# Kernel optimization log

Hardware: AMD Instinct MI355X
Metric: run time of the kernel (lower is better)

The kernel has to match this reference:

```python
import jax, jax.numpy as jnp
import numpy as np
from jax import lax

KERNEL_SIZE = 3  # matches init_kwargs


def setup_inputs() -> dict:
    key = jax.random.key(0)
    heatmap = jax.random.normal(key, (8, 16, 512, 512), dtype=jnp.float32)
    return {"heatmap": heatmap, "max_peaks": 262144}


def reference(heatmap, max_peaks):
    """Peak detection: local maxima of 3x3 neighborhood that are > 0.

    Returns:
      peaks:  (B, max_peaks, 3) float32, rows [x, y, confidence] packed in
              (channel, row-major) order (identical ordering to the torch
              per-channel torch.where + cat), zero-padded after counts[b].
      counts: (B,) int32, number of valid peak rows per batch item.
    """
    k = KERNEL_SIZE
    pad = (k - 1) // 2
    # max_pool2d(stride=1, padding=pad) pads with -inf implicitly
    max_pooled = lax.reduce_window(
        heatmap, -jnp.inf, lax.max,
        window_dimensions=(1, 1, k, k),
        window_strides=(1, 1, 1, 1),
        padding=[(0, 0), (0, 0), (pad, pad), (pad, pad)],
    )
    peak_mask = (heatmap == max_pooled) & (heatmap > 0)

    B, C, H, W = heatmap.shape
    n = C * H * W
    flat_mask = peak_mask.reshape(B, n)
    flat_val = heatmap.reshape(B, n)

    # Stream compaction: stable argsort moves valid flat indices (in order)
    # to the front; invalid entries get sentinel key n.
    idx = jnp.arange(n, dtype=jnp.int32)
    keys = jnp.where(flat_mask, idx, jnp.int32(n))
    order = jnp.argsort(keys, axis=1)[:, :max_peaks]  # (B, max_peaks)

    valid = jnp.take_along_axis(flat_mask, order, axis=1)
    conf = jnp.take_along_axis(flat_val, order, axis=1)
    x = (order % W).astype(heatmap.dtype)
    y = ((order // W) % H).astype(heatmap.dtype)

    peaks = jnp.where(valid[..., None], jnp.stack([x, y, conf], axis=-1), 0.0)
    counts = flat_mask.sum(axis=1).astype(jnp.int32)
    return peaks, counts
```

## Files before the change

### kernel.cpp

```cpp
#include <hip/hip_runtime.h>


namespace {
constexpr int kB = 8;
constexpr int kC = 16;
constexpr int kH = 512;
constexpr int kW = 512;
constexpr int kNPB = kC * kH * kW;
constexpr int kMaxPeaks = 262144;
constexpr int kRows = 8;
constexpr int kStripsPerBatch = kC * (kH / kRows);
constexpr int kNStrips = kB * kStripsPerBatch;
constexpr int kWPB = 4;
constexpr int kTPB = 64 * kWPB;
constexpr int kCap = kRows * kW;
constexpr long long kPeaksElems = (long long)kB * kMaxPeaks * 3;
constexpr float kNeg = -3.402823466e38f;
}

__device__ __forceinline__ float fmax3(float a, float b, float c) {
  return fmaxf(fmaxf(a, b), c);
}

__device__ __forceinline__ void loadrow(const float* __restrict__ rp, int y0,
                                        int i, float d[8]) {
  const int yy = y0 + i;
  if (yy >= 0 && yy < kH) {
    const float4 q0 = *reinterpret_cast<const float4*>(rp + i * kW);
    const float4 q1 = *reinterpret_cast<const float4*>(rp + i * kW + 4);
    d[0] = q0.x; d[1] = q0.y; d[2] = q0.z; d[3] = q0.w;
    d[4] = q1.x; d[5] = q1.y; d[6] = q1.z; d[7] = q1.w;
  } else {
#pragma unroll
    for (int j = 0; j < 8; ++j) d[j] = kNeg;
  }
}


__global__ void __launch_bounds__(kTPB)
peak_record_kernel(const float* __restrict__ hm,
                   unsigned long long* __restrict__ rec,
                   int* __restrict__ cnts) {
  const int t = threadIdx.x, lane = t & 63, wv = t >> 6;
  const int s = blockIdx.x * kWPB + wv;
  const int b = s >> 10;
  const int si = s & 1023;
  const int c = si >> 6;
  const int y0 = (si & 63) * kRows;
  const float* rp = hm + (long long)b * kNPB + c * (kH * kW) + y0 * kW + lane * 8;
  unsigned long long* rb = rec + (long long)s * kCap;

  float A[8], Bv[8], Cv[8], N1[8], N2[8];
  loadrow(rp, y0, -1, A);
  loadrow(rp, y0, 0, Bv);
  loadrow(rp, y0, 1, Cv);
  loadrow(rp, y0, 2, N1);
  loadrow(rp, y0, 3, N2);

  const unsigned long long pm = (lane == 0) ? 0ull : (~0ull >> (64 - lane));
  int rbase = 0;
#pragma unroll
  for (int r = 0; r < kRows; ++r) {
    float cm[8];
#pragma unroll
    for (int j = 0; j < 8; ++j) cm[j] = fmax3(A[j], Bv[j], Cv[j]);
    float hl = __shfl_up(cm[7], 1, 64);
    float hr = __shfl_down(cm[0], 1, 64);
    if (lane == 0) hl = kNeg;
    if (lane == 63) hr = kNeg;
    float m[8];
    m[0] = fmax3(hl, cm[0], cm[1]);
#pragma unroll
    for (int j = 1; j < 7; ++j) m[j] = fmax3(cm[j - 1], cm[j], cm[j + 1]);
    m[7] = fmax3(cm[6], cm[7], hr);

    unsigned long long w[8];
    int lexcl = 0, rowcnt = 0;
#pragma unroll
    for (int j = 0; j < 8; ++j) {
      const float v = Bv[j];
      w[j] = __ballot((v == m[j]) && (v > 0.0f));
      lexcl += (int)__popcll(w[j] & pm);
      rowcnt += (int)__popcll(w[j]);
    }
    int rank = rbase + lexcl;
    const unsigned yx = (unsigned)((y0 + r) << 16);
#pragma unroll
    for (int j = 0; j < 8; ++j) {
      const int f = (int)((w[j] >> lane) & 1);
      if (f) {
        rb[rank] = ((unsigned long long)__float_as_uint(Bv[j]) << 32) |
                   (unsigned long long)(yx | (unsigned)(lane * 8 + j));
      }
      rank += f;
    }
    rbase += rowcnt;

#pragma unroll
    for (int j = 0; j < 8; ++j) { A[j] = Bv[j]; Bv[j] = Cv[j]; Cv[j] = N1[j]; N1[j] = N2[j]; }
    if (r <= 4) loadrow(rp, y0, r + 4, N2);
  }
  if (lane == 0) cnts[s] = rbase;
}

__global__ void __launch_bounds__(kTPB)
peak_scatter_kernel(const unsigned long long* __restrict__ rec,
                    const int* __restrict__ cnts,
                    float* __restrict__ out) {
  __shared__ int s_pre[kWPB], s_tot[kWPB], s_c[kWPB];
  const int t = threadIdx.x, lane = t & 63, wv = t >> 6;
  const int g = blockIdx.x;
  const int b = g >> 8;
  const int g0 = (g & 255) * kWPB;
  const int* cb = cnts + b * kStripsPerBatch;

  const int4 c4 = *reinterpret_cast<const int4*>(cb + t * 4);
  const int idx0 = t * 4;
  int tot = c4.x + c4.y + c4.z + c4.w;
  int pre = (idx0 < g0) ? tot : 0;
  if (idx0 == g0) { s_c[0] = c4.x; s_c[1] = c4.y; s_c[2] = c4.z; s_c[3] = c4.w; }
#pragma unroll
  for (int d = 32; d >= 1; d >>= 1) {
    pre += __shfl_down(pre, d, 64);
    tot += __shfl_down(tot, d, 64);
  }
  if (lane == 0) { s_pre[wv] = pre; s_tot[wv] = tot; }
  __syncthreads();
  const int base = s_pre[0] + s_pre[1] + s_pre[2] + s_pre[3];
  if (g0 == 0 && t == 0)
    out[kPeaksElems + b] =
        (float)(s_tot[0] + s_tot[1] + s_tot[2] + s_tot[3]);

  int off0 = base;
  for (int k = 0; k < wv; ++k) off0 += s_c[k];
  if (off0 >= kMaxPeaks) return;

  const int s = b * kStripsPerBatch + g0 + wv;
  const int lim = min(s_c[wv], kMaxPeaks - off0);
  const unsigned long long* rb = rec + (long long)s * kCap;
  float* o = out + (long long)b * kMaxPeaks * 3 + (long long)off0 * 3;
  for (int i = lane; i < lim; i += 64) {
    const unsigned long long v = rb[i];
    float* p = o + (long long)i * 3;
    p[0] = (float)(unsigned)(v & 0xffffu);
    p[1] = (float)(unsigned)((v >> 16) & 0xffffu);
    p[2] = __uint_as_float((unsigned)(v >> 32));
  }
}


__global__ void __launch_bounds__(kTPB)
peak_count_kernel(const float* __restrict__ hm,
                  unsigned long long* __restrict__ bmw,
                  int* __restrict__ cnts) {
  const int t = threadIdx.x, lane = t & 63, wv = t >> 6;
  const int s = blockIdx.x * kWPB + wv;
  const int b = s >> 10;
  const int si = s & 1023;
  const int c = si >> 6;
  const int y0 = (si & 63) * kRows;
  const float* rp = hm + (long long)b * kNPB + c * (kH * kW) + y0 * kW + lane * 8;

  float A[8], Bv[8], Cv[8], N1[8], N2[8];
  loadrow(rp, y0, -1, A);
  loadrow(rp, y0, 0, Bv);
  loadrow(rp, y0, 1, Cv);
  loadrow(rp, y0, 2, N1);
  loadrow(rp, y0, 3, N2);

  unsigned long long myword = 0;
  int scnt = 0;
#pragma unroll
  for (int r = 0; r < kRows; ++r) {
    float cm[8];
#pragma unroll
    for (int j = 0; j < 8; ++j) cm[j] = fmax3(A[j], Bv[j], Cv[j]);
    float hl = __shfl_up(cm[7], 1, 64);
    float hr = __shfl_down(cm[0], 1, 64);
    if (lane == 0) hl = kNeg;
    if (lane == 63) hr = kNeg;
    float m[8];
    m[0] = fmax3(hl, cm[0], cm[1]);
#pragma unroll
    for (int j = 1; j < 7; ++j) m[j] = fmax3(cm[j - 1], cm[j], cm[j + 1]);
    m[7] = fmax3(cm[6], cm[7], hr);
#pragma unroll
    for (int j = 0; j < 8; ++j) {
      const float v = Bv[j];
      const unsigned long long wj = __ballot((v == m[j]) && (v > 0.0f));
      scnt += (int)__popcll(wj);
      if (lane == r * 8 + j) myword = wj;
    }
#pragma unroll
    for (int j = 0; j < 8; ++j) { A[j] = Bv[j]; Bv[j] = Cv[j]; Cv[j] = N1[j]; N1[j] = N2[j]; }
    if (r <= 4) loadrow(rp, y0, r + 4, N2);
  }
  bmw[(long long)s * 64 + lane] = myword;
  if (lane == 0) cnts[s] = scnt;
}

__global__ void __launch_bounds__(kTPB)
peak_write_kernel(const float* __restrict__ hm,
                  const unsigned long long* __restrict__ bmw,
                  const int* __restrict__ cnts,
                  float* __restrict__ out) {
  __shared__ int s_pre[kWPB], s_tot[kWPB], s_c[kWPB];
  __shared__ unsigned long long s_w[kWPB][64];
  const int t = threadIdx.x, lane = t & 63, wv = t >> 6;
  const int g = blockIdx.x;
  const int b = g >> 8;
  const int g0 = (g & 255) * kWPB;
  const int* cb = cnts + b * kStripsPerBatch;

  const int4 c4 = *reinterpret_cast<const int4*>(cb + t * 4);
  const int idx0 = t * 4;
  int tot = c4.x + c4.y + c4.z + c4.w;
  int pre = (idx0 < g0) ? tot : 0;
  if (idx0 == g0) { s_c[0] = c4.x; s_c[1] = c4.y; s_c[2] = c4.z; s_c[3] = c4.w; }
#pragma unroll
  for (int d = 32; d >= 1; d >>= 1) {
    pre += __shfl_down(pre, d, 64);
    tot += __shfl_down(tot, d, 64);
  }
  if (lane == 0) { s_pre[wv] = pre; s_tot[wv] = tot; }
  __syncthreads();
  const int base = s_pre[0] + s_pre[1] + s_pre[2] + s_pre[3];
  if (g0 == 0 && t == 0)
    out[kPeaksElems + b] =
        (float)(s_tot[0] + s_tot[1] + s_tot[2] + s_tot[3]);

  int off0 = base;
  for (int k = 0; k < wv; ++k) off0 += s_c[k];
  if (off0 >= kMaxPeaks) return;

  const int s = b * kStripsPerBatch + g0 + wv;
  const int si = g0 + wv, c = si >> 6, y0 = (si & 63) * kRows;
  const float* rp = hm + (long long)b * kNPB + c * (kH * kW) + y0 * kW + lane * 8;

  s_w[wv][lane] = bmw[(long long)s * 64 + lane];

  float P0[8], P1[8], cur[8];
  loadrow(rp, y0, 0, P0);
  loadrow(rp, y0, 1, P1);

  const unsigned long long pm = (lane == 0) ? 0ull : (~0ull >> (64 - lane));
  int rbase = off0;
  float* pb = out + (long long)b * kMaxPeaks * 3;
#pragma unroll
  for (int r = 0; r < kRows; ++r) {
#pragma unroll
    for (int j = 0; j < 8; ++j) { cur[j] = P0[j]; P0[j] = P1[j]; }
    if (r < kRows - 2) loadrow(rp, y0, r + 2, P1);

    unsigned long long w[8];
#pragma unroll
    for (int j = 0; j < 8; ++j) w[j] = s_w[wv][r * 8 + j];
    int lexcl = 0, rowcnt = 0;
#pragma unroll
    for (int j = 0; j < 8; ++j) {
      lexcl += (int)__popcll(w[j] & pm);
      rowcnt += (int)__popcll(w[j]);
    }
    int rank = rbase + lexcl;
    const float fy = (float)(y0 + r);
#pragma unroll
    for (int j = 0; j < 8; ++j) {
      const int f = (int)((w[j] >> lane) & 1);
      if (f && rank < kMaxPeaks) {
        float* o = pb + (long long)rank * 3;
        o[0] = (float)(lane * 8 + j);
        o[1] = fy;
        o[2] = cur[j];
      }
      rank += f;
    }
    rbase += rowcnt;
    if (rbase >= kMaxPeaks) break;
  }
}

extern "C" void kernel_launch(void* const* d_in, const int* in_sizes, int n_in,
                              void* d_out, int out_size, void* d_ws, size_t ws_size,
                              hipStream_t stream) {
  const float* hm = (const float*)d_in[0];
  float* out = (float*)d_out;

  const size_t rec_bytes =
      (size_t)kNStrips * (size_t)kCap * sizeof(unsigned long long);
  const size_t need = rec_bytes + (size_t)kNStrips * sizeof(int);

  if (ws_size >= need) {
    unsigned long long* rec = (unsigned long long*)d_ws;
    int* cnts = (int*)((char*)d_ws + rec_bytes);
    peak_record_kernel<<<kNStrips / kWPB, kTPB, 0, stream>>>(hm, rec, cnts);
    peak_scatter_kernel<<<kNStrips / kWPB, kTPB, 0, stream>>>(rec, cnts, out);
  } else {
    unsigned long long* bmw = (unsigned long long*)d_ws;
    int* cnts = (int*)(bmw + (long long)kNStrips * 64);
    peak_count_kernel<<<kNStrips / kWPB, kTPB, 0, stream>>>(hm, bmw, cnts);
    peak_write_kernel<<<kNStrips / kWPB, kTPB, 0, stream>>>(hm, bmw, cnts, out);
  }
}
```

Baseline: 219.3 us.

## Fuse peak record and scatter into one cooperative kernel with grid sync

Merges the record and scatter kernels into one cooperative launch that uses a grid-wide sync between them, so one kernel launch and the second kernel's reload of state go away. Strips grow to 16 rows, which halves the grid to 1024 blocks so every block can be co-resident, as a grid sync requires. Rows of halo reloaded per strip shrink as well. If the cooperative launch fails, it falls back to the old two-kernel path. The grid sync adds its own cost, and fewer, longer waves may lower memory-level parallelism.

```diff
diff --git a/kernel.cpp b/kernel.cpp
--- a/kernel.cpp
+++ b/kernel.cpp
@@ -1,4 +1,5 @@
 #include <hip/hip_runtime.h>
+#include <hip/hip_cooperative_groups.h>
 
 
 namespace {
@@ -8,14 +9,20 @@
 constexpr int kW = 512;
 constexpr int kNPB = kC * kH * kW;
 constexpr int kMaxPeaks = 262144;
+constexpr long long kPeaksElems = (long long)kB * kMaxPeaks * 3;
+constexpr float kNeg = -3.402823466e38f;
+constexpr int kWPB = 4;
+constexpr int kTPB = 64 * kWPB;
+
+constexpr int kRows16 = 16;
+constexpr int kS16PerBatch = kC * (kH / kRows16);
+constexpr int kNS16 = kB * kS16PerBatch;
+constexpr int kCap16 = kRows16 * kW;
+
 constexpr int kRows = 8;
 constexpr int kStripsPerBatch = kC * (kH / kRows);
 constexpr int kNStrips = kB * kStripsPerBatch;
-constexpr int kWPB = 4;
-constexpr int kTPB = 64 * kWPB;
 constexpr int kCap = kRows * kW;
-constexpr long long kPeaksElems = (long long)kB * kMaxPeaks * 3;
-constexpr float kNeg = -3.402823466e38f;
 }
 
 __device__ __forceinline__ float fmax3(float a, float b, float c) {
@@ -36,6 +43,110 @@
   }
 }
 
+__global__ void __launch_bounds__(kTPB, 4)
+peak_fused_kernel(const float* __restrict__ hm,
+                  unsigned long long* __restrict__ rec,
+                  int* __restrict__ cnts,
+                  float* __restrict__ out) {
+  const int t = threadIdx.x, lane = t & 63, wv = t >> 6;
+  const int g = blockIdx.x;
+  const int b = g >> 7;
+  const int g0 = (g & 127) * kWPB;
+  const int si = g0 + wv;
+  const int s = b * kS16PerBatch + si;
+  const int c = si >> 5;
+  const int y0 = (si & 31) * kRows16;
+  const float* rp = hm + (long long)b * kNPB + c * (kH * kW) + y0 * kW + lane * 8;
+  unsigned long long* rb = rec + (long long)s * kCap16;
+
+  float A[8], Bv[8], Cv[8], N1[8], N2[8];
+  loadrow(rp, y0, -1, A);
+  loadrow(rp, y0, 0, Bv);
+  loadrow(rp, y0, 1, Cv);
+  loadrow(rp, y0, 2, N1);
+  loadrow(rp, y0, 3, N2);
+
+  const unsigned long long pm = (lane == 0) ? 0ull : (~0ull >> (64 - lane));
+  int rbase = 0;
+#pragma unroll
+  for (int r = 0; r < kRows16; ++r) {
+    float cm[8];
+#pragma unroll
+    for (int j = 0; j < 8; ++j) cm[j] = fmax3(A[j], Bv[j], Cv[j]);
+    float hl = __shfl_up(cm[7], 1, 64);
+    float hr = __shfl_down(cm[0], 1, 64);
+    if (lane == 0) hl = kNeg;
+    if (lane == 63) hr = kNeg;
+    float m[8];
+    m[0] = fmax3(hl, cm[0], cm[1]);
+#pragma unroll
+    for (int j = 1; j < 7; ++j) m[j] = fmax3(cm[j - 1], cm[j], cm[j + 1]);
+    m[7] = fmax3(cm[6], cm[7], hr);
+
+    unsigned long long w[8];
+    int lexcl = 0, rowcnt = 0;
+#pragma unroll
+    for (int j = 0; j < 8; ++j) {
+      const float v = Bv[j];
+      w[j] = __ballot((v == m[j]) && (v > 0.0f));
+      lexcl += (int)__popcll(w[j] & pm);
+      rowcnt += (int)__popcll(w[j]);
+    }
+    int rank = rbase + lexcl;
+    const unsigned yx = (unsigned)((y0 + r) << 16);
+#pragma unroll
+    for (int j = 0; j < 8; ++j) {
+      const int f = (int)((w[j] >> lane) & 1);
+      if (f) {
+        rb[rank] = ((unsigned long long)__float_as_uint(Bv[j]) << 32) |
+                   (unsigned long long)(yx | (unsigned)(lane * 8 + j));
+      }
+      rank += f;
+    }
+    rbase += rowcnt;
+
+#pragma unroll
+    for (int j = 0; j < 8; ++j) { A[j] = Bv[j]; Bv[j] = Cv[j]; Cv[j] = N1[j]; N1[j] = N2[j]; }
+    if (r <= kRows16 - 4) loadrow(rp, y0, r + 4, N2);
+  }
+  if (lane == 0) cnts[s] = rbase;
+
+  cooperative_groups::this_grid().sync();
+
+  __shared__ int s_pre[kWPB], s_tot[kWPB], s_c[kWPB];
+  const int* cb = cnts + b * kS16PerBatch;
+  const int2 c2 = *reinterpret_cast<const int2*>(cb + t * 2);
+  const int idx0 = t * 2;
+  int tot = c2.x + c2.y;
+  int pre = (idx0 < g0) ? tot : 0;
+  if (idx0 == g0)     { s_c[0] = c2.x; s_c[1] = c2.y; }
+  if (idx0 == g0 + 2) { s_c[2] = c2.x; s_c[3] = c2.y; }
+#pragma unroll
+  for (int d = 32; d >= 1; d >>= 1) {
+    pre += __shfl_down(pre, d, 64);
+    tot += __shfl_down(tot, d, 64);
+  }
+  if (lane == 0) { s_pre[wv] = pre; s_tot[wv] = tot; }
+  __syncthreads();
+  const int base = s_pre[0] + s_pre[1] + s_pre[2] + s_pre[3];
+  if (g0 == 0 && t == 0)
+    out[kPeaksElems + b] =
+        (float)(s_tot[0] + s_tot[1] + s_tot[2] + s_tot[3]);
+
+  int off0 = base;
+  for (int k = 0; k < wv; ++k) off0 += s_c[k];
+  if (off0 >= kMaxPeaks) return;
+
+  const int lim = min(s_c[wv], kMaxPeaks - off0);
+  float* o = out + (long long)b * kMaxPeaks * 3 + (long long)off0 * 3;
+  for (int i = lane; i < lim; i += 64) {
+    const unsigned long long v = rb[i];
+    float* p = o + (long long)i * 3;
+    p[0] = (float)(unsigned)(v & 0xffffu);
+    p[1] = (float)(unsigned)((v >> 16) & 0xffffu);
+    p[2] = __uint_as_float((unsigned)(v >> 32));
+  }
+}
 
 __global__ void __launch_bounds__(kTPB)
 peak_record_kernel(const float* __restrict__ hm,
@@ -95,7 +206,6 @@
       rank += f;
     }
     rbase += rowcnt;
-
 #pragma unroll
     for (int j = 0; j < 8; ++j) { A[j] = Bv[j]; Bv[j] = Cv[j]; Cv[j] = N1[j]; N1[j] = N2[j]; }
     if (r <= 4) loadrow(rp, y0, r + 4, N2);
@@ -147,7 +257,6 @@
     p[2] = __uint_as_float((unsigned)(v >> 32));
   }
 }
-
 
 __global__ void __launch_bounds__(kTPB)
 peak_count_kernel(const float* __restrict__ hm,
@@ -286,14 +395,21 @@
   float* out = (float*)d_out;
 
   const size_t rec_bytes =
-      (size_t)kNStrips * (size_t)kCap * sizeof(unsigned long long);
-  const size_t need = rec_bytes + (size_t)kNStrips * sizeof(int);
+      (size_t)kNS16 * (size_t)kCap16 * sizeof(unsigned long long);
+  const size_t need = rec_bytes + (size_t)kNS16 * sizeof(int);
 
   if (ws_size >= need) {
     unsigned long long* rec = (unsigned long long*)d_ws;
     int* cnts = (int*)((char*)d_ws + rec_bytes);
-    peak_record_kernel<<<kNStrips / kWPB, kTPB, 0, stream>>>(hm, rec, cnts);
-    peak_scatter_kernel<<<kNStrips / kWPB, kTPB, 0, stream>>>(rec, cnts, out);
+    void* args[4] = {(void*)&hm, (void*)&rec, (void*)&cnts, (void*)&out};
+    hipError_t e = hipLaunchCooperativeKernel(
+        (void*)peak_fused_kernel, dim3(kNS16 / kWPB), dim3(kTPB), args, 0,
+        stream);
+    if (e != hipSuccess) {
+      (void)hipGetLastError();
+      peak_record_kernel<<<kNStrips / kWPB, kTPB, 0, stream>>>(hm, rec, cnts);
+      peak_scatter_kernel<<<kNStrips / kWPB, kTPB, 0, stream>>>(rec, cnts, out);
+    }
   } else {
     unsigned long long* bmw = (unsigned long long*)d_ws;
     int* cnts = (int*)(bmw + (long long)kNStrips * 64);
```

After: 383.6 us. +74.9%, slower.
